# Optimization experiments

Hardware: AMD Instinct MI355X
Metric: run time of the kernel (lower is better)

The kernel has to match this reference:

```python
import jax, jax.numpy as jnp
import numpy as np

HID = 1280; HEADS = 16; HEAD_DIM = 80; INTER = 3456; DEPTH = 6
MERGE = 2; UNIT = 4; PATCH = 16; WIN = 128; OUT_DIM = 2048
T, H, W = 1, 128, 128
N = T * H * W                       # 16384 patch tokens
ROT_DIM = HEAD_DIM // 2             # 40
VITW = WIN // MERGE // PATCH        # 4 llm positions per window side
WIN_TOK = VITW * VITW * MERGE * MERGE  # 64 tokens per attention window
DEEPSTACK = (2, 4)
EPS = 1e-6


def setup_inputs() -> dict:
    key = jax.random.key(0)
    ks = jax.random.split(key, 24)
    p = lambda k, shape: jax.random.normal(k, shape, jnp.float32) * 0.02

    # --- rotary position ids (faithful to _rot_pos_emb), host-side numpy ---
    hp = np.arange(H)[:, None].repeat(W, 1)
    wp = np.arange(W)[None, :].repeat(H, 0)
    hp = hp.reshape(H // MERGE, MERGE, W // MERGE, MERGE).transpose(0, 2, 1, 3).reshape(-1)
    wp = wp.reshape(H // MERGE, MERGE, W // MERGE, MERGE).transpose(0, 2, 1, 3).reshape(-1)
    pos = np.stack([hp, wp], -1)                       # [N, 2] (t=1)
    inv_freq = 1.0 / (10000.0 ** (np.arange(ROT_DIM) / ROT_DIM))
    freqs = np.outer(np.arange(max(H, W)), inv_freq)   # [128, 40]
    rpe = freqs[pos].reshape(N, -1)                    # [N, 80] == head_dim
    cos = jnp.asarray(np.cos(rpe), jnp.float32)
    sin = jnp.asarray(np.sin(rpe), jnp.float32)

    # --- window index (faithful to _get_window_index; no padding needed) ---
    lh, lw = H // MERGE, W // MERGE                    # 64, 64
    idx = np.arange(T * lh * lw).reshape(T, lh, lw)
    idx = idx.reshape(T, lh // VITW, VITW, lw // VITW, VITW).transpose(0, 1, 3, 2, 4).reshape(-1)
    window_index = jnp.asarray(idx, jnp.int32)         # [N // UNIT] = [4096]

    return {
        'pixel_values': jax.random.normal(ks[0], (N, 1536), jnp.float32),
        'cos': cos, 'sin': sin, 'window_index': window_index,
        'W_patch': p(ks[1], (1536, HID)),
        'norm1_w': jnp.ones((DEPTH, HID), jnp.float32),
        'qkv_w': p(ks[2], (DEPTH, HID, 3 * HID)),
        'qkv_b': jnp.zeros((DEPTH, 3 * HID), jnp.float32),
        'proj_w': p(ks[3], (DEPTH, HID, HID)),
        'proj_b': jnp.zeros((DEPTH, HID), jnp.float32),
        'norm2_w': jnp.ones((DEPTH, HID), jnp.float32),
        'gate_w': p(ks[4], (DEPTH, HID, INTER)),
        'gate_b': jnp.zeros((DEPTH, INTER), jnp.float32),
        'up_w': p(ks[5], (DEPTH, HID, INTER)),
        'up_b': jnp.zeros((DEPTH, INTER), jnp.float32),
        'down_w': p(ks[6], (DEPTH, INTER, HID)),
        'down_b': jnp.zeros((DEPTH, HID), jnp.float32),
        'm_norm_w': jnp.ones((HID,), jnp.float32),
        'm_l1_w': p(ks[7], (UNIT * HID, UNIT * HID)),
        'm_l1_b': jnp.zeros((UNIT * HID,), jnp.float32),
        'm_l2_w': p(ks[8], (UNIT * HID, OUT_DIM)),
        'm_l2_b': jnp.zeros((OUT_DIM,), jnp.float32),
        'd_norm_w': jnp.ones((2, UNIT * HID), jnp.float32),
        'd_l1_w': p(ks[9], (2, UNIT * HID, UNIT * HID)),
        'd_l1_b': jnp.zeros((2, UNIT * HID), jnp.float32),
        'd_l2_w': p(ks[10], (2, UNIT * HID, OUT_DIM)),
        'd_l2_b': jnp.zeros((2, OUT_DIM), jnp.float32),
    }


def _rms(x, w):
    return x * jax.lax.rsqrt(jnp.mean(x * x, -1, keepdims=True) + EPS) * w


def _rotate_half(x):
    x1, x2 = jnp.split(x, 2, -1)
    return jnp.concatenate([-x2, x1], -1)


def _attn(x, cos, sin, wqkv, bqkv, wp, bp):
    n = x.shape[0]
    q, k, v = jnp.split(x @ wqkv + bqkv, 3, -1)
    q = q.reshape(n, HEADS, HEAD_DIM)
    k = k.reshape(n, HEADS, HEAD_DIM)
    v = v.reshape(n, HEADS, HEAD_DIM)
    c, s = cos[:, None, :], sin[:, None, :]
    q = q * c + _rotate_half(q) * s
    k = k * c + _rotate_half(k) * s
    nw = n // WIN_TOK  # equal-size windows -> batched window attention (same math as per-window loop)
    qw = q.reshape(nw, WIN_TOK, HEADS, HEAD_DIM)
    kw = k.reshape(nw, WIN_TOK, HEADS, HEAD_DIM)
    vw = v.reshape(nw, WIN_TOK, HEADS, HEAD_DIM)
    scores = jnp.einsum('wqhd,wkhd->whqk', qw, kw) * (HEAD_DIM ** -0.5)
    probs = jax.nn.softmax(scores, -1)
    out = jnp.einsum('whqk,wkhd->wqhd', probs, vw).reshape(n, HID)
    return out @ wp + bp


def _merger(h, norm_w, l1w, l1b, l2w, l2b, postshuffle):
    if postshuffle:
        x = _rms(h.reshape(-1, UNIT * HID), norm_w)
    else:
        x = _rms(h, norm_w).reshape(-1, UNIT * HID)
    return jax.nn.gelu(x @ l1w + l1b) @ l2w + l2b


def reference(pixel_values, cos, sin, window_index, W_patch, norm1_w, qkv_w, qkv_b,
              proj_w, proj_b, norm2_w, gate_w, gate_b, up_w, up_b, down_w, down_b,
              m_norm_w, m_l1_w, m_l1_b, m_l2_w, m_l2_b,
              d_norm_w, d_l1_w, d_l1_b, d_l2_w, d_l2_b):
    h = pixel_values @ W_patch                                  # patch embed [N, HID]
    # reorder tokens into window order at merge-unit granularity
    h = h.reshape(-1, UNIT, HID)[window_index].reshape(-1, HID)
    cos_r = cos.reshape(-1, UNIT, HEAD_DIM)[window_index].reshape(-1, HEAD_DIM)
    sin_r = sin.reshape(-1, UNIT, HEAD_DIM)[window_index].reshape(-1, HEAD_DIM)

    deep = []
    for i in range(DEPTH):
        h = h + _attn(_rms(h, norm1_w[i]), cos_r, sin_r, qkv_w[i], qkv_b[i], proj_w[i], proj_b[i])
        x = _rms(h, norm2_w[i])
        h = h + (jax.nn.silu(x @ gate_w[i] + gate_b[i]) * (x @ up_w[i] + up_b[i])) @ down_w[i] + down_b[i]
        if i in DEEPSTACK:
            j = DEEPSTACK.index(i)
            deep.append(_merger(h, d_norm_w[j], d_l1_w[j], d_l1_b[j], d_l2_w[j], d_l2_b[j], True))

    merged = _merger(h, m_norm_w, m_l1_w, m_l1_b, m_l2_w, m_l2_b, False)
    rev = jnp.argsort(window_index)                             # restore original order
    outs = [merged[rev]] + [d[rev] for d in deep]
    return jnp.stack(outs, 0)                                   # [3, N//UNIT, OUT_DIM]
```

## Files before the change

### kernel.cpp

```cpp
#include <hip/hip_runtime.h>
#include <hip/hip_bf16.h>

typedef unsigned short u16;
typedef __bf16 bf16x8 __attribute__((ext_vector_type(8)));
typedef float   f32x4 __attribute__((ext_vector_type(4)));
typedef unsigned short u16x8 __attribute__((ext_vector_type(8)));

#define NTOK  16384
#define HID_  1280
#define NHEAD 16
#define HD    80
#define INTER_ 3456
#define NGRP  4096
#define ODIM  2048
#define BIGD  5120

static __device__ __forceinline__ u16 f2bf(float f) {
  __hip_bfloat16 h = __float2bfloat16(f);
  return __builtin_bit_cast(u16, h);
}
static __device__ __forceinline__ float bf2f(u16 u) {
  return __bfloat162float(__builtin_bit_cast(__hip_bfloat16, u));
}
static __device__ __forceinline__ float gelu_tanh(float x) {
  float y = 0.7978845608028654f * (x + 0.044715f * x * x * x);
  float t = 1.0f - 2.0f / (1.0f + __expf(2.0f * y));
  return 0.5f * x * (1.0f + t);
}

static __device__ __forceinline__ void gload_lds16(const u16* g, u16* l) {
  __builtin_amdgcn_global_load_lds(
      (const __attribute__((address_space(1))) unsigned int*)g,
      (__attribute__((address_space(3))) unsigned int*)l, 16, 0, 0);
}

__global__ __launch_bounds__(256) void gather_pv_k(
    const float* __restrict__ pv, const int* __restrict__ wi, u16* __restrict__ out) {
  int t = blockIdx.x * 256 + threadIdx.x;
  if (t >= NTOK * 384) return;
  int i = t / 384, c4 = t - i * 384;
  int s = wi[i >> 2] * 4 + (i & 3);
  float4 v = *(const float4*)(pv + (size_t)s * 1536 + c4 * 4);
  uint2 r;
  r.x = (unsigned)f2bf(v.x) | ((unsigned)f2bf(v.y) << 16);
  r.y = (unsigned)f2bf(v.z) | ((unsigned)f2bf(v.w) << 16);
  *(uint2*)(out + (size_t)i * 1536 + c4 * 4) = r;
}

__global__ __launch_bounds__(256) void gather_cs_k(
    const float* __restrict__ ci, const float* __restrict__ si,
    const int* __restrict__ wi, float* __restrict__ co, float* __restrict__ so) {
  int t = blockIdx.x * 256 + threadIdx.x;
  if (t >= NTOK * 20) return;
  int i = t / 20, c4 = t - i * 20;
  int s = wi[i >> 2] * 4 + (i & 3);
  *(float4*)(co + (size_t)i * 80 + c4 * 4) = *(const float4*)(ci + (size_t)s * 80 + c4 * 4);
  *(float4*)(so + (size_t)i * 80 + c4 * 4) = *(const float4*)(si + (size_t)s * 80 + c4 * 4);
}

__global__ __launch_bounds__(256) void twt_k(
    const float* __restrict__ W, u16* __restrict__ Wt, int K, int N) {
  __shared__ u16 t[32][33];
  int bn = blockIdx.x * 32, bk = blockIdx.y * 32;
  int tx = threadIdx.x & 31, ty = threadIdx.x >> 5;
  #pragma unroll
  for (int r = 0; r < 4; r++) {
    int k = bk + ty + r * 8;
    t[tx][ty + r * 8] = f2bf(W[(size_t)k * N + bn + tx]);
  }
  __syncthreads();
  #pragma unroll
  for (int r = 0; r < 4; r++) {
    int n = bn + ty + r * 8;
    Wt[(size_t)n * K + bk + tx] = t[ty + r * 8][tx];
  }
}

__global__ __launch_bounds__(256) void rmsnorm_k(
    const float* __restrict__ x, const float* __restrict__ w, u16* __restrict__ out, int D) {
  int row = blockIdx.x;
  const float* xr = x + (size_t)row * D;
  float ss = 0.f;
  for (int c = threadIdx.x; c < D; c += 256) { float v = xr[c]; ss += v * v; }
  #pragma unroll
  for (int d = 1; d < 64; d <<= 1) ss += __shfl_xor(ss, d, 64);
  __shared__ float part[4];
  if ((threadIdx.x & 63) == 0) part[threadIdx.x >> 6] = ss;
  __syncthreads();
  float tot = part[0] + part[1] + part[2] + part[3];
  float scale = rsqrtf(tot / (float)D + 1e-6f);
  u16* orow = out + (size_t)row * D;
  for (int c = threadIdx.x; c < D; c += 256) orow[c] = f2bf(xr[c] * scale * w[c]);
}

template <int MODE, int TM>
__global__ __launch_bounds__(512, 2) void gemm8_k(
    const u16* __restrict__ A, const u16* __restrict__ Bt, const float* __restrict__ bias,
    void* __restrict__ outp, const int* __restrict__ rowmap, const u16* __restrict__ gatebuf,
    int nbn, int N, int K) {
  constexpr int MF = TM / 64;
  constexpr unsigned ABUFSZ = (unsigned)TM * 128u;
  constexpr int NBUF = (TM == 256) ? 2 : 3;
  constexpr unsigned BBASE = (unsigned)NBUF * ABUFSZ;
  __shared__ __align__(16) u16 LDS[(TM == 256) ? 65536 : 73728];
  const int tid = threadIdx.x;
  const int w = tid >> 6, lane = tid & 63;
  const int wm = w >> 2, wn = w & 3;
  const int lr = lane & 15, lk = lane >> 4, lrm = lr & 7;
  const int NT = K >> 6;
  const size_t Kb = (size_t)K * 2;
  const int l8 = lane >> 3, l7 = lane & 7;
  const int schunk = l7 ^ l8;

  const int nwg = gridDim.x;
  const int q8 = nwg >> 3, r8 = nwg & 7;
  const int xcd = blockIdx.x & 7, ord = blockIdx.x >> 3;
  const int id = (xcd < r8 ? xcd * (q8 + 1) : r8 * (q8 + 1) + (xcd - r8) * q8) + ord;
  const int bn = id % nbn, bm = id / nbn;

  const unsigned wm16lr = (unsigned)(wm * 16 + lr) * 128u;
  const unsigned wn16lr = (unsigned)(wn * 16 + lr) * 128u;
  unsigned ch[2];
  ch[0] = (unsigned)(((lk) ^ lrm) << 4);
  ch[1] = (unsigned)(((4 + lk) ^ lrm) << 4);
  const char* LB = (const char*)&LDS[0];

  f32x4 acc[2 * MF][4];
  #pragma unroll
  for (int f = 0; f < 2 * MF; f++)
    #pragma unroll
    for (int n = 0; n < 4; n++) { acc[f][n][0]=0.f; acc[f][n][1]=0.f; acc[f][n][2]=0.f; acc[f][n][3]=0.f; }

  const char* Ab = (const char*)A;
  const char* Bb = (const char*)Bt;
  u16* LDSp = &LDS[0];

  bf16x8 afE[MF][2], afO[MF][2], bfE[2][2], bfO[2][2];

  auto STAGE = [&](int isB, int half, int tt, int bb) {
    long k0b = (long)tt * 128;
    if (!isB) {
      if constexpr (TM == 256) {
        int rb = bm * 256 + half * 128;
        #pragma unroll
        for (int i = 0; i < 2; i++) {
          int r0 = half * 128 + i * 64 + w * 8;
          int gr = rb + i * 64 + w * 8 + l8;
          const char* src = Ab + (size_t)gr * Kb + k0b + schunk * 16;
          unsigned dst = (unsigned)bb * ABUFSZ + (unsigned)r0 * 128u;
          gload_lds16((const u16*)src, LDSp + dst / 2);
        }
      } else {
        int r0 = half * 64 + w * 8;
        int gr = bm * 128 + half * 64 + w * 8 + l8;
        const char* src = Ab + (size_t)gr * Kb + k0b + schunk * 16;
        unsigned dst = (unsigned)bb * ABUFSZ + (unsigned)r0 * 128u;
        gload_lds16((const u16*)src, LDSp + dst / 2);
      }
    } else {
      int rb = bn * 256 + half * 128;
      #pragma unroll
      for (int i = 0; i < 2; i++) {
        int r0 = half * 128 + i * 64 + w * 8;
        int gr = rb + i * 64 + w * 8 + l8;
        if (gr >= N) gr = N - 1;
        const char* src = Bb + (size_t)gr * Kb + k0b + schunk * 16;
        unsigned dst = BBASE + (unsigned)bb * 32768u + (unsigned)r0 * 128u;
        gload_lds16((const u16*)src, LDSp + dst / 2);
      }
    }
  };

#define QREAD_A(DST, MH, ABUF)                                                      \
    _Pragma("unroll") for (int f = 0; f < MF; f++) {                                \
      _Pragma("unroll") for (int kk = 0; kk < 2; kk++) {                            \
        unsigned ad = (ABUF) + (unsigned)((MH) * MF + f) * 4096u + wm16lr + ch[kk]; \
        DST[f][kk] = *(const bf16x8*)(LB + ad);                                     \
      }                                                                             \
    }

#define QREAD_B(DST, NH, BBUF)                                                      \
    _Pragma("unroll") for (int n = 0; n < 2; n++) {                                 \
      _Pragma("unroll") for (int kk = 0; kk < 2; kk++) {                            \
        unsigned ad = BBASE + (BBUF) + (unsigned)((NH) * 2 + n) * 8192u + wn16lr + ch[kk]; \
        DST[n][kk] = *(const bf16x8*)(LB + ad);                                     \
      }                                                                             \
    }

#define QMFMA(AF, BF, MH, NH)                                                       \
    __builtin_amdgcn_s_setprio(1);                                                  \
    _Pragma("unroll") for (int kk = 0; kk < 2; kk++) {                              \
      _Pragma("unroll") for (int f = 0; f < MF; f++) {                              \
        _Pragma("unroll") for (int n = 0; n < 2; n++) {                             \
          acc[(MH) * MF + f][(NH) * 2 + n] = __builtin_amdgcn_mfma_f32_16x16x32_bf16( \
              AF[f][kk], BF[n][kk], acc[(MH) * MF + f][(NH) * 2 + n], 0, 0, 0);     \
        }                                                                           \
      }                                                                             \
    }                                                                               \
    __builtin_amdgcn_s_setprio(0);

#define SYNC1(VM)                                                                   \
    asm volatile("s_waitcnt vmcnt(" #VM ")" ::: "memory");                          \
    __builtin_amdgcn_s_barrier();                                                   \
    asm volatile("s_waitcnt lgkmcnt(0)" ::: "memory");                              \
    __builtin_amdgcn_sched_barrier(0);

#define LGKM0                                                                       \
    asm volatile("s_waitcnt lgkmcnt(0)" ::: "memory");                              \
    __builtin_amdgcn_sched_barrier(0);

#define SYNC2                                                                       \
    __builtin_amdgcn_s_barrier();                                                   \
    __builtin_amdgcn_sched_barrier(0);

  if constexpr (TM == 256) {
    STAGE(0, 0, 0, 0);
    STAGE(1, 0, 0, 0);
    STAGE(0, 1, 0, 0);
    STAGE(1, 1, 0, 0);
    for (int t = 0; t < NT; t++) {
      const unsigned aob  = (unsigned)(t & 1) * ABUFSZ;
      const unsigned bob  = (unsigned)(t & 1) * 32768u;
      const int bb1 = (t + 1) & 1;
      const int tn = (t + 1 < NT) ? (t + 1) : 0;
      {
        STAGE(0, 0, tn, bb1);
        SYNC1(6)
        if (t > 0) { QMFMA(afO, bfO, 1, 1) }
        SYNC2
      }
      {
        QREAD_A(afE, 0, aob)
        QREAD_B(bfE, 0, bob)
        STAGE(1, 0, tn, bb1);
        SYNC1(6)
        QMFMA(afE, bfE, 0, 0)
        SYNC2
      }
      {
        QREAD_A(afO, 1, aob)
        STAGE(0, 1, tn, bb1);
        SYNC1(6)
        QMFMA(afO, bfE, 1, 0)
        SYNC2
      }
      {
        QREAD_B(bfO, 1, bob)
        STAGE(1, 1, tn, bb1);
        SYNC1(6)
        QMFMA(afE, bfO, 0, 1)
        SYNC2
      }
    }
    QMFMA(afO, bfO, 1, 1)
  } else {
    STAGE(0, 0, 0, 0);
    STAGE(1, 0, 0, 0);
    STAGE(0, 1, 0, 0);
    STAGE(1, 1, 0, 0);
    STAGE(0, 0, 1, 1);
    STAGE(1, 0, 1, 1);
    STAGE(0, 1, 1, 1);
    STAGE(1, 1, 1, 1);
    asm volatile("s_waitcnt vmcnt(6)" ::: "memory");
    __builtin_amdgcn_s_barrier();
    __builtin_amdgcn_sched_barrier(0);
    int cb = 0;
    for (int t = 0; t < NT; t++) {
      const unsigned aob = (unsigned)cb * ABUFSZ;
      const unsigned bob = (unsigned)cb * 32768u;
      int sb = cb + 2; if (sb >= 3) sb -= 3;
      const int tn = (t + 2 < NT) ? (t + 2) : t;
      QREAD_A(afE, 0, aob)
      QREAD_A(afO, 1, aob)
      QREAD_B(bfE, 0, bob)
      STAGE(0, 0, tn, sb);
      STAGE(1, 0, tn, sb);
      LGKM0
      QMFMA(afE, bfE, 0, 0)
      QMFMA(afO, bfE, 1, 0)
      QREAD_B(bfO, 1, bob)
      STAGE(0, 1, tn, sb);
      STAGE(1, 1, tn, sb);
      asm volatile("s_waitcnt vmcnt(6)" ::: "memory");
      __builtin_amdgcn_s_barrier();
      LGKM0
      QMFMA(afE, bfO, 0, 1)
      QMFMA(afO, bfO, 1, 1)
      SYNC2
      cb++; if (cb == 3) cb = 0;
    }
  }
#undef QREAD_A
#undef QREAD_B
#undef QMFMA
#undef SYNC1
#undef LGKM0
#undef SYNC2

  #pragma unroll
  for (int nf = 0; nf < 4; nf++) {
    int Cc = bn * 256 + nf * 64 + wn * 16 + lr;
    bool ok = (Cc < N);
    float bv = (bias && ok) ? bias[Cc] : 0.f;
    #pragma unroll
    for (int mf = 0; mf < 2 * MF; mf++) {
      #pragma unroll
      for (int j = 0; j < 4; j++) {
        int R = bm * TM + mf * 32 + wm * 16 + lk * 4 + j;
        float v = acc[mf][nf][j] + bv;
        if (ok) {
          if (MODE == 0) {
            ((u16*)outp)[(size_t)R * N + Cc] = f2bf(v);
          } else if (MODE == 1) {
            ((float*)outp)[(size_t)R * N + Cc] = v;
          } else if (MODE == 2) {
            ((float*)outp)[(size_t)R * N + Cc] += v;
          } else if (MODE == 3) {
            ((u16*)outp)[(size_t)R * N + Cc] = f2bf(gelu_tanh(v));
          } else if (MODE == 4) {
            int orow = rowmap[R];
            ((float*)outp)[(size_t)orow * N + Cc] = v;
          } else {
            float g = bf2f(gatebuf[(size_t)R * N + Cc]);
            float sg = g / (1.f + __expf(-g));
            ((u16*)outp)[(size_t)R * N + Cc] = f2bf(sg * v);
          }
        }
      }
    }
  }
}

__global__ __launch_bounds__(256, 2) void attn_k(
    const u16* __restrict__ qkv, u16* __restrict__ outO,
    const float* __restrict__ cosr, const float* __restrict__ sinr) {
  __shared__ u16 Qs[64 * 104];
  __shared__ u16 Ks[64 * 104];
  __shared__ u16 Vt[80 * 72];
  __shared__ u16 Ps[64 * 72];
  const int w = blockIdx.x, hd = blockIdx.y;
  const int tid = threadIdx.x;
  const u16* base = qkv + (size_t)w * 64 * 3840 + hd * 80;

  for (int idx = tid; idx < 64 * 96; idx += 256) {
    int r = idx / 96, c = idx - r * 96;
    u16 qv = 0, kv = 0;
    if (c < 80) {
      int tokg = w * 64 + r;
      float cc = cosr[(size_t)tokg * 80 + c], ss = sinr[(size_t)tokg * 80 + c];
      int cp = (c < 40) ? c + 40 : c - 40;
      float sgn = (c < 40) ? -1.f : 1.f;
      float q  = bf2f(base[(size_t)r * 3840 + c]);
      float qp = bf2f(base[(size_t)r * 3840 + cp]);
      float k  = bf2f(base[(size_t)r * 3840 + 1280 + c]);
      float kp = bf2f(base[(size_t)r * 3840 + 1280 + cp]);
      qv = f2bf(q * cc + sgn * qp * ss);
      kv = f2bf(k * cc + sgn * kp * ss);
    }
    Qs[r * 104 + c] = qv;
    Ks[r * 104 + c] = kv;
  }
  for (int idx = tid; idx < 80 * 64; idx += 256) {
    int d = idx >> 6, kt = idx & 63;
    Vt[d * 72 + kt] = base[(size_t)kt * 3840 + 2560 + d];
  }
  __syncthreads();

  const int lane = tid & 63, wv = tid >> 6;
  const int lr = lane & 15, lk = lane >> 4;
  const float sc = 0.11180339887498949f;

  f32x4 sfrag[4];
  #pragma unroll
  for (int f = 0; f < 4; f++) { sfrag[f][0]=0.f; sfrag[f][1]=0.f; sfrag[f][2]=0.f; sfrag[f][3]=0.f; }
  bf16x8 aq[3];
  #pragma unroll
  for (int ks = 0; ks < 3; ks++) aq[ks] = *(const bf16x8*)&Qs[(wv * 16 + lr) * 104 + ks * 32 + lk * 8];
  #pragma unroll
  for (int fn = 0; fn < 4; fn++) {
    #pragma unroll
    for (int ks = 0; ks < 3; ks++) {
      bf16x8 bk = *(const bf16x8*)&Ks[(fn * 16 + lr) * 104 + ks * 32 + lk * 8];
      sfrag[fn] = __builtin_amdgcn_mfma_f32_16x16x32_bf16(aq[ks], bk, sfrag[fn], 0, 0, 0);
    }
  }

  float inv[4];
  #pragma unroll
  for (int j = 0; j < 4; j++) {
    float mx = -1e30f;
    #pragma unroll
    for (int fn = 0; fn < 4; fn++) mx = fmaxf(mx, sfrag[fn][j] * sc);
    #pragma unroll
    for (int d = 1; d < 16; d <<= 1) mx = fmaxf(mx, __shfl_xor(mx, d, 64));
    float sum = 0.f;
    #pragma unroll
    for (int fn = 0; fn < 4; fn++) {
      float e = __expf(sfrag[fn][j] * sc - mx);
      Ps[(wv * 16 + lk * 4 + j) * 72 + fn * 16 + lr] = f2bf(e);
      sum += e;
    }
    #pragma unroll
    for (int d = 1; d < 16; d <<= 1) sum += __shfl_xor(sum, d, 64);
    inv[j] = 1.0f / sum;
  }
  __syncthreads();

  bf16x8 ap[2];
  #pragma unroll
  for (int ks = 0; ks < 2; ks++) ap[ks] = *(const bf16x8*)&Ps[(wv * 16 + lr) * 72 + ks * 32 + lk * 8];
  f32x4 of[5];
  #pragma unroll
  for (int f = 0; f < 5; f++) { of[f][0]=0.f; of[f][1]=0.f; of[f][2]=0.f; of[f][3]=0.f; }
  #pragma unroll
  for (int fn2 = 0; fn2 < 5; fn2++) {
    #pragma unroll
    for (int ks = 0; ks < 2; ks++) {
      bf16x8 bv = *(const bf16x8*)&Vt[(fn2 * 16 + lr) * 72 + ks * 32 + lk * 8];
      of[fn2] = __builtin_amdgcn_mfma_f32_16x16x32_bf16(ap[ks], bv, of[fn2], 0, 0, 0);
    }
  }

  #pragma unroll
  for (int fn2 = 0; fn2 < 5; fn2++) {
    #pragma unroll
    for (int j = 0; j < 4; j++) {
      int q = wv * 16 + lk * 4 + j;
      int d = fn2 * 16 + lr;
      outO[((size_t)(w * 64 + q)) * 1280 + hd * 80 + d] = f2bf(of[fn2][j] * inv[j]);
    }
  }
}

extern "C" void kernel_launch(void* const* d_in, const int* in_sizes, int n_in,
                              void* d_out, int out_size, void* d_ws, size_t ws_size,
                              hipStream_t stream) {
  (void)in_sizes; (void)n_in; (void)out_size; (void)ws_size;
  const float* pv   = (const float*)d_in[0];
  const float* cosi = (const float*)d_in[1];
  const float* sini = (const float*)d_in[2];
  const int*   wi   = (const int*)d_in[3];
  const float* Wp   = (const float*)d_in[4];
  const float* n1w  = (const float*)d_in[5];
  const float* qkvw = (const float*)d_in[6];
  const float* qkvb = (const float*)d_in[7];
  const float* pw   = (const float*)d_in[8];
  const float* pb   = (const float*)d_in[9];
  const float* n2w  = (const float*)d_in[10];
  const float* gw   = (const float*)d_in[11];
  const float* gb   = (const float*)d_in[12];
  const float* uw   = (const float*)d_in[13];
  const float* ub   = (const float*)d_in[14];
  const float* dw   = (const float*)d_in[15];
  const float* db   = (const float*)d_in[16];
  const float* mnw  = (const float*)d_in[17];
  const float* ml1w = (const float*)d_in[18];
  const float* ml1b = (const float*)d_in[19];
  const float* ml2w = (const float*)d_in[20];
  const float* ml2b = (const float*)d_in[21];
  const float* dnw  = (const float*)d_in[22];
  const float* dl1w = (const float*)d_in[23];
  const float* dl1b = (const float*)d_in[24];
  const float* dl2w = (const float*)d_in[25];
  const float* dl2b = (const float*)d_in[26];
  float* outv = (float*)d_out;
  char* ws = (char*)d_ws;

  size_t off = 0;
  float* h    = (float*)(ws + off); off += (size_t)NTOK * HID_ * 4;
  float* cosr = (float*)(ws + off); off += (size_t)NTOK * 80 * 4;
  float* sinr = (float*)(ws + off); off += (size_t)NTOK * 80 * 4;
  u16*  xb    = (u16*)(ws + off);  off += (size_t)NTOK * HID_ * 2;
  u16*  bufA  = (u16*)(ws + off);  off += (size_t)NTOK * 3840 * 2;
  u16*  bufB  = (u16*)(ws + off);  off += (size_t)NTOK * INTER_ * 2;
  u16*  bufC  = (u16*)(ws + off);  off += (size_t)NTOK * HID_ * 2;
  u16*  Wt    = (u16*)(ws + off);  off += (size_t)BIGD * BIGD * 2;

  dim3 B256(256), B512(512);
  #define TW(src, K_, N_) twt_k<<<dim3((N_) / 32, (K_) / 32), B256, 0, stream>>>((src), Wt, (K_), (N_))
  #define G8(MODE, TM_, Abuf, bias_, out_, rmap_, gate_, M_, N_, K_)                      \
    gemm8_k<MODE, TM_><<<dim3(((M_) / (TM_)) * (((N_) + 255) / 256)), B512, 0, stream>>>( \
        (Abuf), Wt, (bias_), (out_), (rmap_), (gate_), (((N_) + 255) / 256), (N_), (K_))

  gather_pv_k<<<(NTOK * 384 + 255) / 256, B256, 0, stream>>>(pv, wi, bufA);
  gather_cs_k<<<(NTOK * 20 + 255) / 256, B256, 0, stream>>>(cosi, sini, wi, cosr, sinr);

  TW(Wp, 1536, HID_);
  G8(1, 128, bufA, nullptr, h, nullptr, nullptr, NTOK, HID_, 1536);

  for (int i = 0; i < 6; i++) {
    rmsnorm_k<<<NTOK, B256, 0, stream>>>(h, n1w + (size_t)i * HID_, xb, HID_);
    TW(qkvw + (size_t)i * HID_ * 3840, HID_, 3840);
    G8(0, 256, xb, qkvb + (size_t)i * 3840, bufA, nullptr, nullptr, NTOK, 3840, HID_);
    attn_k<<<dim3(256, 16), B256, 0, stream>>>(bufA, bufC, cosr, sinr);
    TW(pw + (size_t)i * HID_ * HID_, HID_, HID_);
    G8(2, 128, bufC, pb + (size_t)i * HID_, h, nullptr, nullptr, NTOK, HID_, HID_);
    rmsnorm_k<<<NTOK, B256, 0, stream>>>(h, n2w + (size_t)i * HID_, xb, HID_);
    TW(gw + (size_t)i * HID_ * INTER_, HID_, INTER_);
    G8(0, 256, xb, gb + (size_t)i * INTER_, bufB, nullptr, nullptr, NTOK, INTER_, HID_);
    TW(uw + (size_t)i * HID_ * INTER_, HID_, INTER_);
    G8(5, 256, xb, ub + (size_t)i * INTER_, bufA, nullptr, bufB, NTOK, INTER_, HID_);
    TW(dw + (size_t)i * INTER_ * HID_, INTER_, HID_);
    G8(2, 128, bufA, db + (size_t)i * HID_, h, nullptr, nullptr, NTOK, HID_, INTER_);
    if (i == 2 || i == 4) {
      int j = (i == 2) ? 0 : 1;
      rmsnorm_k<<<NGRP, B256, 0, stream>>>(h, dnw + (size_t)j * BIGD, bufC, BIGD);
      TW(dl1w + (size_t)j * BIGD * BIGD, BIGD, BIGD);
      G8(3, 128, bufC, dl1b + (size_t)j * BIGD, bufA, nullptr, nullptr, NGRP, BIGD, BIGD);
      TW(dl2w + (size_t)j * BIGD * ODIM, BIGD, ODIM);
      G8(4, 128, bufA, dl2b + (size_t)j * ODIM, outv + (size_t)(1 + j) * NGRP * ODIM,
         wi, nullptr, NGRP, ODIM, BIGD);
    }
  }

  rmsnorm_k<<<NTOK, B256, 0, stream>>>(h, mnw, bufC, HID_);
  TW(ml1w, BIGD, BIGD);
  G8(3, 128, bufC, ml1b, bufA, nullptr, nullptr, NGRP, BIGD, BIGD);
  TW(ml2w, BIGD, ODIM);
  G8(4, 128, bufA, ml2b, outv, wi, nullptr, NGRP, ODIM, BIGD);
  #undef TW
  #undef G8
}
```

Measured before the change: 8.007 ms.

## Fuse gate and up projections into one interleaved GEMM with SwiGLU epilogue

Interleaves the gate and up weight columns (and biases) so a single GEMM of width 2*INTER computes both projections. The epilogue pairs adjacent columns with a lane shuffle and writes silu(gate)*up directly, so the bf16 gate intermediate is never written or read back. This removes one GEMM launch, one pass over the activation input, and a full gate-buffer round trip through memory. The cost is a wider GEMM tile grid, extra weight-transpose launches, and half the lanes idle during the epilogue store.

```diff
diff --git a/kernel.cpp b/kernel.cpp
--- a/kernel.cpp
+++ b/kernel.cpp
@@ -74,6 +74,30 @@
     int n = bn + ty + r * 8;
     Wt[(size_t)n * K + bk + tx] = t[ty + r * 8][tx];
   }
+}
+
+__global__ __launch_bounds__(256) void twt2_k(
+    const float* __restrict__ W, u16* __restrict__ Wt, int K, int N, int ph) {
+  __shared__ u16 t[32][33];
+  int bn = blockIdx.x * 32, bk = blockIdx.y * 32;
+  int tx = threadIdx.x & 31, ty = threadIdx.x >> 5;
+  #pragma unroll
+  for (int r = 0; r < 4; r++) {
+    int k = bk + ty + r * 8;
+    t[tx][ty + r * 8] = f2bf(W[(size_t)k * N + bn + tx]);
+  }
+  __syncthreads();
+  #pragma unroll
+  for (int r = 0; r < 4; r++) {
+    int n = bn + ty + r * 8;
+    Wt[(size_t)(2 * n + ph) * K + bk + tx] = t[ty + r * 8][tx];
+  }
+}
+
+__global__ __launch_bounds__(256) void bi_k(
+    const float* __restrict__ g, const float* __restrict__ u, float* __restrict__ o, int n) {
+  int i = blockIdx.x * 256 + threadIdx.x;
+  if (i < n) { o[2 * i] = g[i]; o[2 * i + 1] = u[i]; }
 }
 
 __global__ __launch_bounds__(256) void rmsnorm_k(
@@ -309,7 +333,13 @@
       for (int j = 0; j < 4; j++) {
         int R = bm * TM + mf * 32 + wm * 16 + lk * 4 + j;
         float v = acc[mf][nf][j] + bv;
-        if (ok) {
+        if (MODE == 6) {
+          float vp = __shfl_xor(v, 1, 64);
+          if ((lr & 1) == 0) {
+            float s = v / (1.f + __expf(-v));
+            ((u16*)outp)[(size_t)R * (N >> 1) + (Cc >> 1)] = f2bf(s * vp);
+          }
+        } else if (ok) {
           if (MODE == 0) {
             ((u16*)outp)[(size_t)R * N + Cc] = f2bf(v);
           } else if (MODE == 1) {
@@ -321,10 +351,6 @@
           } else if (MODE == 4) {
             int orow = rowmap[R];
             ((float*)outp)[(size_t)orow * N + Cc] = v;
-          } else {
-            float g = bf2f(gatebuf[(size_t)R * N + Cc]);
-            float sg = g / (1.f + __expf(-g));
-            ((u16*)outp)[(size_t)R * N + Cc] = f2bf(sg * v);
           }
         }
       }
@@ -476,6 +502,7 @@
   u16*  bufB  = (u16*)(ws + off);  off += (size_t)NTOK * INTER_ * 2;
   u16*  bufC  = (u16*)(ws + off);  off += (size_t)NTOK * HID_ * 2;
   u16*  Wt    = (u16*)(ws + off);  off += (size_t)BIGD * BIGD * 2;
+  float* ibuf = (float*)(ws + off); off += (size_t)2 * INTER_ * 4;
 
   dim3 B256(256), B512(512);
   #define TW(src, K_, N_) twt_k<<<dim3((N_) / 32, (K_) / 32), B256, 0, stream>>>((src), Wt, (K_), (N_))
@@ -497,10 +524,13 @@
     TW(pw + (size_t)i * HID_ * HID_, HID_, HID_);
     G8(2, 128, bufC, pb + (size_t)i * HID_, h, nullptr, nullptr, NTOK, HID_, HID_);
     rmsnorm_k<<<NTOK, B256, 0, stream>>>(h, n2w + (size_t)i * HID_, xb, HID_);
-    TW(gw + (size_t)i * HID_ * INTER_, HID_, INTER_);
-    G8(0, 256, xb, gb + (size_t)i * INTER_, bufB, nullptr, nullptr, NTOK, INTER_, HID_);
-    TW(uw + (size_t)i * HID_ * INTER_, HID_, INTER_);
-    G8(5, 256, xb, ub + (size_t)i * INTER_, bufA, nullptr, bufB, NTOK, INTER_, HID_);
+    twt2_k<<<dim3(INTER_ / 32, HID_ / 32), B256, 0, stream>>>(
+        gw + (size_t)i * HID_ * INTER_, Wt, HID_, INTER_, 0);
+    twt2_k<<<dim3(INTER_ / 32, HID_ / 32), B256, 0, stream>>>(
+        uw + (size_t)i * HID_ * INTER_, Wt, HID_, INTER_, 1);
+    bi_k<<<(INTER_ + 255) / 256, B256, 0, stream>>>(
+        gb + (size_t)i * INTER_, ub + (size_t)i * INTER_, ibuf, INTER_);
+    G8(6, 256, xb, ibuf, bufA, nullptr, nullptr, NTOK, 2 * INTER_, HID_);
     TW(dw + (size_t)i * INTER_ * HID_, INTER_, HID_);
     G8(2, 128, bufA, db + (size_t)i * HID_, h, nullptr, nullptr, NTOK, HID_, INTER_);
     if (i == 2 || i == 4) {
```

Result: faster. 7.634 ms (-4.7%).
